# Kernel tuning notes

Hardware: AMD Instinct MI355X
Metric: run time of the kernel (lower is better)

## Reference

```python
import jax, jax.numpy as jnp
import numpy as np

B, SQ, SK, D, H = 2, 2048, 2048, 1024, 16
DK = D // H


def setup_inputs() -> dict:
    key = jax.random.key(0)
    ks = jax.random.split(key, 9)
    query = jax.random.normal(ks[0], (B, SQ, D), dtype=jnp.float32)
    k_in = jax.random.normal(ks[1], (B, SK, D), dtype=jnp.float32)
    v_in = jax.random.normal(ks[2], (B, SK, D), dtype=jnp.float32)
    # padding mask: 1 for valid tokens, 0 for padding; lengths in [SK//2, SK]
    lengths = jax.random.randint(ks[3], (B,), SK // 2, SK + 1)
    mask = (jnp.arange(SK)[None, :] < lengths[:, None]).astype(jnp.int32)
    scale = 1.0 / np.sqrt(D)
    Wq = jax.random.normal(ks[4], (D, D), dtype=jnp.float32) * scale
    Wk = jax.random.normal(ks[5], (D, D), dtype=jnp.float32) * scale
    Wv = jax.random.normal(ks[6], (D, D), dtype=jnp.float32) * scale
    Wo = jax.random.normal(ks[7], (D, D), dtype=jnp.float32) * scale
    return {"query": query, "key": k_in, "value": v_in, "mask": mask,
            "Wq": Wq, "Wk": Wk, "Wv": Wv, "Wo": Wo}


def reference(query, key, value, mask, Wq, Wk, Wv, Wo):
    # linear projections (torch Linear: x @ W.T)
    q = (query @ Wq.T).reshape(B, SQ, H, DK).transpose(0, 2, 1, 3)  # [B,H,SQ,DK]
    k = (key @ Wk.T).reshape(B, SK, H, DK).transpose(0, 2, 1, 3)    # [B,H,SK,DK]
    v = (value @ Wv.T).reshape(B, SK, H, DK).transpose(0, 2, 1, 3)  # [B,H,SK,DK]
    scores = jnp.einsum('bhqd,bhkd->bhqk', q, k) / jnp.sqrt(jnp.float32(DK))
    # padding mask: (B, SK) -> (B, 1, 1, SK)
    scores = jnp.where(mask[:, None, None, :] == 0, -jnp.inf, scores)
    # future (causal) mask
    future = jnp.triu(jnp.ones((SQ, SK), dtype=bool), k=1)
    scores = jnp.where(future[None, None], -jnp.inf, scores)
    attn = jax.nn.softmax(scores, axis=-1)
    attn = jnp.nan_to_num(attn, nan=0.0)
    ctx = jnp.einsum('bhqk,bhkd->bhqd', attn, v)
    ctx = ctx.transpose(0, 2, 1, 3).reshape(B, SQ, D)
    return ctx @ Wo.T
```

## Files before the change

### kernel.cpp

```cpp
#include <hip/hip_runtime.h>
#include <hip/hip_bf16.h>
#include <stdint.h>

#define BB 2
#define SS 2048
#define DD 1024
#define HH 16
#define DKK 64
#define MM (BB*SS)
#define LOG2E 1.4426950408889634f
#define QSCALE (0.125f * LOG2E)

typedef __attribute__((ext_vector_type(8))) short short8;
typedef __attribute__((ext_vector_type(4))) float f32x4;

__device__ __forceinline__ short bfr(float f) {
    return (short)((__float_as_uint(f) + 0x8000u) >> 16);
}

__device__ __forceinline__ short8 cvt8(float4 a, float4 b) {
    short8 s;
    s[0] = bfr(a.x); s[1] = bfr(a.y); s[2] = bfr(a.z); s[3] = bfr(a.w);
    s[4] = bfr(b.x); s[5] = bfr(b.y); s[6] = bfr(b.z); s[7] = bfr(b.w);
    return s;
}

__global__ __launch_bounds__(256) void qkv_gemm(const float* __restrict__ Aq,
                                                const float* __restrict__ Ak,
                                                const float* __restrict__ Av,
                                                const float* __restrict__ Wq,
                                                const float* __restrict__ Wk,
                                                const float* __restrict__ Wv,
                                                short* __restrict__ Qb,
                                                short* __restrict__ Kb,
                                                short* __restrict__ Vtb) {
    __shared__ __align__(16) short As[2][128][40];
    __shared__ __align__(16) short Ws[2][128][40];
    const int z = blockIdx.z;
    const float* A = (z == 0) ? Aq : (z == 1) ? Ak : Av;
    const float* W = (z == 0) ? Wq : (z == 1) ? Wk : Wv;
    short* Y = (z == 0) ? Qb : (z == 1) ? Kb : Vtb;

    const int t    = threadIdx.x;
    const int wave = t >> 6;
    const int lane = t & 63;
    const int la   = lane & 15;
    const int quad = lane >> 4;
    const int wm   = wave & 1;
    const int wn   = wave >> 1;
    const int m0   = blockIdx.x * 128;
    const int n0   = blockIdx.y * 128;

    const int srow = t >> 1;
    const int scol = (t & 1) * 16;

    f32x4 acc[4][4];
    #pragma unroll
    for (int i = 0; i < 4; ++i)
        #pragma unroll
        for (int j = 0; j < 4; ++j) acc[i][j] = {0.f, 0.f, 0.f, 0.f};

    float4 ar[4], wr[4];
    auto loadG = [&](int i) {
        const int k0 = i * 32;
        const float4* pa = (const float4*)(A + (size_t)(m0 + srow) * DD + k0 + scol);
        ar[0] = pa[0]; ar[1] = pa[1]; ar[2] = pa[2]; ar[3] = pa[3];
        const float4* pw = (const float4*)(W + (size_t)(n0 + srow) * DD + k0 + scol);
        wr[0] = pw[0]; wr[1] = pw[1]; wr[2] = pw[2]; wr[3] = pw[3];
    };
    auto storeL = [&](int buf) {
        *(short8*)&As[buf][srow][scol]     = cvt8(ar[0], ar[1]);
        *(short8*)&As[buf][srow][scol + 8] = cvt8(ar[2], ar[3]);
        *(short8*)&Ws[buf][srow][scol]     = cvt8(wr[0], wr[1]);
        *(short8*)&Ws[buf][srow][scol + 8] = cvt8(wr[2], wr[3]);
    };

    loadG(0);
    storeL(0);
    __syncthreads();

    const int NIT = DD / 32;
    for (int i = 0; i < NIT; ++i) {
        if (i + 1 < NIT) loadG(i + 1);
        const int buf = i & 1;
        short8 af[4], bfv[4];
        #pragma unroll
        for (int mt = 0; mt < 4; ++mt)
            af[mt] = *(const short8*)&As[buf][wm * 64 + mt * 16 + la][quad * 8];
        #pragma unroll
        for (int nt = 0; nt < 4; ++nt)
            bfv[nt] = *(const short8*)&Ws[buf][wn * 64 + nt * 16 + la][quad * 8];
        #pragma unroll
        for (int mt = 0; mt < 4; ++mt)
            #pragma unroll
            for (int nt = 0; nt < 4; ++nt)
                acc[mt][nt] = __builtin_amdgcn_mfma_f32_16x16x32_bf16(af[mt], bfv[nt], acc[mt][nt], 0, 0, 0);
        if (i + 1 < NIT) {
            storeL((i + 1) & 1);
            __syncthreads();
        }
    }

    #pragma unroll
    for (int mt = 0; mt < 4; ++mt) {
        #pragma unroll
        for (int nt = 0; nt < 4; ++nt) {
            #pragma unroll
            for (int r = 0; r < 4; ++r) {
                const int m = m0 + wm * 64 + mt * 16 + quad * 4 + r;
                const int n = n0 + wn * 64 + nt * 16 + la;
                const int b = m >> 11, s = m & (SS - 1);
                const int h = n >> 6,  dk = n & (DKK - 1);
                float v = acc[mt][nt][r];
                if (z == 0) {
                    Y[(((size_t)(b * HH + h) * SS + s) * DKK) + dk] = bfr(v * QSCALE);
                } else if (z == 1) {
                    Y[(((size_t)(b * HH + h) * SS + s) * DKK) + dk] = bfr(v);
                } else {
                    Y[(((size_t)(b * HH + h) * DKK + dk) * SS) + s] = bfr(v);
                }
            }
        }
    }
}

__global__ __launch_bounds__(256) void attn_fused(const short* __restrict__ Q,
                                                  const short* __restrict__ K,
                                                  const short* __restrict__ Vt,
                                                  const int* __restrict__ mask,
                                                  short* __restrict__ ctx) {
    const int b = blockIdx.z, h = blockIdx.y, x = blockIdx.x;
    const int t = threadIdx.x, wave = t >> 6, lane = t & 63;
    const int la = lane & 15, quad = lane >> 4;

    __shared__ __align__(16) short Ks[2][64][72];
    __shared__ __align__(16) short Vs[2][64][72];
    __shared__ __align__(16) short Ps[64][72];

    const size_t kbase = ((size_t)(b * HH + h) * SS) * DKK;
    const size_t vbase = ((size_t)(b * HH + h) * DKK) * SS;

    const int srow = t >> 2;
    const int scol = (t & 3) * 16;
    short8 kr[2], vr[2];

    auto loadG = [&](int kt) {
        const short* kp = K + kbase + (size_t)(kt * 64 + srow) * DKK + scol;
        kr[0] = ((const short8*)kp)[0]; kr[1] = ((const short8*)kp)[1];
        const short* vp = Vt + vbase + (size_t)srow * SS + kt * 64 + scol;
        vr[0] = ((const short8*)vp)[0]; vr[1] = ((const short8*)vp)[1];
    };
    auto storeL = [&](int buf) {
        *(short8*)&Ks[buf][srow][scol]     = kr[0];
        *(short8*)&Ks[buf][srow][scol + 8] = kr[1];
        *(short8*)&Vs[buf][srow][scol]     = vr[0];
        *(short8*)&Vs[buf][srow][scol + 8] = vr[1];
    };

    #pragma unroll 1
    for (int phase = 0; phase < 2; ++phase) {
        const int qt = phase ? x : (31 - x);
        const size_t qbase = kbase + (size_t)(qt * 64) * DKK;
        const short8 aq0 = *(const short8*)(Q + qbase + (size_t)(wave * 16 + la) * DKK + quad * 8);
        const short8 aq1 = *(const short8*)(Q + qbase + (size_t)(wave * 16 + la) * DKK + 32 + quad * 8);

        float rs[4] = {0.f, 0.f, 0.f, 0.f};
        f32x4 o[4];
        #pragma unroll
        for (int dc = 0; dc < 4; ++dc) o[dc] = {0.f, 0.f, 0.f, 0.f};

        const int nkt = qt + 1;
        loadG(0);
        storeL(0);
        __syncthreads();

        for (int kt = 0; kt < nkt; ++kt) {
            if (kt + 1 < nkt) loadG(kt + 1);
            const int buf = kt & 1;
            const bool diag   = (kt == qt);
            const bool padded = (kt >= SS / 128);

            f32x4 s[4];
            #pragma unroll
            for (int ct = 0; ct < 4; ++ct) {
                s[ct] = {0.f, 0.f, 0.f, 0.f};
                short8 kb0 = *(const short8*)&Ks[buf][ct * 16 + la][quad * 8];
                short8 kb1 = *(const short8*)&Ks[buf][ct * 16 + la][32 + quad * 8];
                s[ct] = __builtin_amdgcn_mfma_f32_16x16x32_bf16(aq0, kb0, s[ct], 0, 0, 0);
                s[ct] = __builtin_amdgcn_mfma_f32_16x16x32_bf16(aq1, kb1, s[ct], 0, 0, 0);
            }

            const int rowq = qt * 64 + wave * 16 + quad * 4;
            #pragma unroll
            for (int ct = 0; ct < 4; ++ct) {
                const int col = kt * 64 + ct * 16 + la;
                const int mv = padded ? mask[b * SS + col] : 1;
                #pragma unroll
                for (int r = 0; r < 4; ++r) {
                    const bool dead = (diag && col > rowq + r) || (padded && mv == 0);
                    const float p = dead ? 0.f : exp2f(s[ct][r]);
                    rs[r] += p;
                    Ps[wave * 16 + quad * 4 + r][ct * 16 + la] = bfr(p);
                }
            }

            #pragma unroll
            for (int c2 = 0; c2 < 2; ++c2) {
                short8 pa = *(const short8*)&Ps[wave * 16 + la][c2 * 32 + quad * 8];
                #pragma unroll
                for (int dc = 0; dc < 4; ++dc) {
                    short8 vb = *(const short8*)&Vs[buf][dc * 16 + la][c2 * 32 + quad * 8];
                    o[dc] = __builtin_amdgcn_mfma_f32_16x16x32_bf16(pa, vb, o[dc], 0, 0, 0);
                }
            }

            if (kt + 1 < nkt) {
                storeL((kt + 1) & 1);
                __syncthreads();
            }
        }

        #pragma unroll
        for (int r = 0; r < 4; ++r) {
            float v = rs[r];
            v += __shfl_xor(v, 1, 64);
            v += __shfl_xor(v, 2, 64);
            v += __shfl_xor(v, 4, 64);
            v += __shfl_xor(v, 8, 64);
            const float inv = 1.0f / v;
            const int q = qt * 64 + wave * 16 + quad * 4 + r;
            #pragma unroll
            for (int dc = 0; dc < 4; ++dc) {
                const int d = dc * 16 + la;
                ctx[((size_t)(b * SS + q) * DD) + h * DKK + d] = bfr(o[dc][r] * inv);
            }
        }
        __syncthreads();
    }
}

__global__ __launch_bounds__(256) void o_gemm(const short* __restrict__ Ctx,
                                              const float* __restrict__ Wo,
                                              float* __restrict__ out) {
    __shared__ __align__(16) short As[2][128][40];
    __shared__ __align__(16) short Ws[2][64][40];
    const int t    = threadIdx.x;
    const int wave = t >> 6;
    const int lane = t & 63;
    const int la   = lane & 15;
    const int quad = lane >> 4;
    const int wm   = wave & 1;
    const int wn   = wave >> 1;
    const int m0   = blockIdx.x * 128;
    const int n0   = blockIdx.y * 64;

    const int srowA = t >> 1;
    const int scolA = (t & 1) * 16;
    const int srowW = t >> 2;
    const int scolW = (t & 3) * 8;

    f32x4 acc[4][2];
    #pragma unroll
    for (int i = 0; i < 4; ++i)
        #pragma unroll
        for (int j = 0; j < 2; ++j) acc[i][j] = {0.f, 0.f, 0.f, 0.f};

    short8 ab[2];
    float4 wr[2];
    auto loadG = [&](int i) {
        const int k0 = i * 32;
        const short8* pa = (const short8*)(Ctx + (size_t)(m0 + srowA) * DD + k0 + scolA);
        ab[0] = pa[0]; ab[1] = pa[1];
        const float4* pw = (const float4*)(Wo + (size_t)(n0 + srowW) * DD + k0 + scolW);
        wr[0] = pw[0]; wr[1] = pw[1];
    };
    auto storeL = [&](int buf) {
        *(short8*)&As[buf][srowA][scolA]     = ab[0];
        *(short8*)&As[buf][srowA][scolA + 8] = ab[1];
        *(short8*)&Ws[buf][srowW][scolW]     = cvt8(wr[0], wr[1]);
    };

    loadG(0);
    storeL(0);
    __syncthreads();

    const int NIT = DD / 32;
    for (int i = 0; i < NIT; ++i) {
        if (i + 1 < NIT) loadG(i + 1);
        const int buf = i & 1;
        short8 af[4], bfv[2];
        #pragma unroll
        for (int mt = 0; mt < 4; ++mt)
            af[mt] = *(const short8*)&As[buf][wm * 64 + mt * 16 + la][quad * 8];
        #pragma unroll
        for (int nt = 0; nt < 2; ++nt)
            bfv[nt] = *(const short8*)&Ws[buf][wn * 32 + nt * 16 + la][quad * 8];
        #pragma unroll
        for (int mt = 0; mt < 4; ++mt)
            #pragma unroll
            for (int nt = 0; nt < 2; ++nt)
                acc[mt][nt] = __builtin_amdgcn_mfma_f32_16x16x32_bf16(af[mt], bfv[nt], acc[mt][nt], 0, 0, 0);
        if (i + 1 < NIT) {
            storeL((i + 1) & 1);
            __syncthreads();
        }
    }

    #pragma unroll
    for (int mt = 0; mt < 4; ++mt) {
        #pragma unroll
        for (int nt = 0; nt < 2; ++nt) {
            #pragma unroll
            for (int r = 0; r < 4; ++r) {
                const int m = m0 + wm * 64 + mt * 16 + quad * 4 + r;
                const int n = n0 + wn * 32 + nt * 16 + la;
                out[(size_t)m * DD + n] = acc[mt][nt][r];
            }
        }
    }
}

extern "C" void kernel_launch(void* const* d_in, const int* in_sizes, int n_in,
                              void* d_out, int out_size, void* d_ws, size_t ws_size,
                              hipStream_t stream) {
    (void)in_sizes; (void)n_in; (void)out_size; (void)ws_size;
    const float* query = (const float*)d_in[0];
    const float* key   = (const float*)d_in[1];
    const float* value = (const float*)d_in[2];
    const int*   mask  = (const int*)  d_in[3];
    const float* Wq    = (const float*)d_in[4];
    const float* Wk    = (const float*)d_in[5];
    const float* Wv    = (const float*)d_in[6];
    const float* Wo    = (const float*)d_in[7];

    short* Qb  = (short*)d_ws;
    short* Kb  = Qb + (size_t)BB * HH * SS * DKK;
    short* Vtb = Kb + (size_t)BB * HH * SS * DKK;
    short* Ctx = Vtb + (size_t)BB * HH * SS * DKK;

    dim3 tb(256);

    dim3 gq(MM / 128, DD / 128, 3);
    hipLaunchKernelGGL(qkv_gemm, gq, tb, 0, stream, query, key, value, Wq, Wk, Wv,
                       Qb, Kb, Vtb);

    dim3 ga(SS / 128, HH, BB);
    hipLaunchKernelGGL(attn_fused, ga, tb, 0, stream, (const short*)Qb, (const short*)Kb,
                       (const short*)Vtb, mask, Ctx);

    dim3 go(MM / 128, DD / 64);
    hipLaunchKernelGGL(o_gemm, go, tb, 0, stream, (const short*)Ctx, Wo, (float*)d_out);
}
```

Before: 257.0 us.

## Add bf16 pre-conversion pass and direct global-to-LDS loads with pre-padded K/V tiles

Adds a pass that converts all fp32 activations and weights to bf16 in one sweep. The GEMMs then load tiles straight into LDS with global_load_lds, with no register staging or in-loop conversion. The QKV projection writes K and V in pre-padded 64x72 tile layouts so the attention kernel can copy each tile to LDS directly. Attention now uses 128-thread blocks, each wave handling 32 query rows. The new path drops double buffering and only runs when the workspace is large enough, trading an extra full read and write of the inputs for cheaper inner loops.

```diff
diff --git a/kernel.cpp b/kernel.cpp
--- a/kernel.cpp
+++ b/kernel.cpp
@@ -17,12 +17,279 @@
 __device__ __forceinline__ short bfr(float f) {
     return (short)((__float_as_uint(f) + 0x8000u) >> 16);
 }
-
 __device__ __forceinline__ short8 cvt8(float4 a, float4 b) {
     short8 s;
     s[0] = bfr(a.x); s[1] = bfr(a.y); s[2] = bfr(a.z); s[3] = bfr(a.w);
     s[4] = bfr(b.x); s[5] = bfr(b.y); s[6] = bfr(b.z); s[7] = bfr(b.w);
     return s;
+}
+
+__device__ __forceinline__ void dma16(const void* g, void* l) {
+    __builtin_amdgcn_global_load_lds(
+        (const __attribute__((address_space(1))) uint32_t*)g,
+        (__attribute__((address_space(3))) uint32_t*)(uintptr_t)l, 16, 0, 0);
+}
+
+
+__global__ __launch_bounds__(256) void cvt_all(const float* __restrict__ q,
+                                               const float* __restrict__ k,
+                                               const float* __restrict__ v,
+                                               const float* __restrict__ wq,
+                                               const float* __restrict__ wk,
+                                               const float* __restrict__ wv,
+                                               const float* __restrict__ wo,
+                                               short* __restrict__ dst) {
+    const size_t nth = (size_t)gridDim.x * blockDim.x;
+    const size_t tid = (size_t)blockIdx.x * blockDim.x + threadIdx.x;
+    for (size_t i8 = tid; i8 < (1u << 21); i8 += nth) {
+        const size_t e = i8 * 8;
+        const float* s;
+        size_t rel;
+        if (e < 4194304)        { s = q; rel = e; }
+        else if (e < 8388608)   { s = k; rel = e - 4194304; }
+        else if (e < 12582912)  { s = v; rel = e - 8388608; }
+        else {
+            const size_t we = e - 12582912;
+            s = (we < 1048576) ? wq : (we < 2097152) ? wk : (we < 3145728) ? wv : wo;
+            rel = we & 1048575;
+        }
+        const float4* p = (const float4*)(s + rel);
+        *(short8*)(dst + e) = cvt8(p[0], p[1]);
+    }
+}
+
+__global__ __launch_bounds__(256) void qkv_lds(const short* __restrict__ Abf,
+                                               const short* __restrict__ Wbf,
+                                               short* __restrict__ Qb,
+                                               short* __restrict__ Kp,
+                                               short* __restrict__ Vp) {
+    __shared__ __align__(16) short As[128 * 32];
+    __shared__ __align__(16) short Ws[128 * 32];
+    const int z = blockIdx.z;
+    const short* A = Abf + (size_t)z * 4194304;
+    const short* W = Wbf + (size_t)z * 1048576;
+    const int t = threadIdx.x, wave = t >> 6, lane = t & 63;
+    const int la = lane & 15, quad = lane >> 4;
+    const int wm = wave & 1, wn = wave >> 1;
+    const int m0 = blockIdx.x * 128, n0 = blockIdx.y * 128;
+
+    f32x4 acc[4][4];
+    #pragma unroll
+    for (int i = 0; i < 4; ++i)
+        #pragma unroll
+        for (int j = 0; j < 4; ++j) acc[i][j] = {0.f, 0.f, 0.f, 0.f};
+
+    const int c0 = t, c1 = 256 + t;
+
+    for (int k0 = 0; k0 < DD; k0 += 32) {
+        dma16(A + (size_t)(m0 + (c0 >> 2)) * DD + k0 + (c0 & 3) * 8, (short*)As + c0 * 8);
+        dma16(A + (size_t)(m0 + (c1 >> 2)) * DD + k0 + (c1 & 3) * 8, (short*)As + c1 * 8);
+        dma16(W + (size_t)(n0 + (c0 >> 2)) * DD + k0 + (c0 & 3) * 8, (short*)Ws + c0 * 8);
+        dma16(W + (size_t)(n0 + (c1 >> 2)) * DD + k0 + (c1 & 3) * 8, (short*)Ws + c1 * 8);
+        __syncthreads();
+        short8 af[4], bf[4];
+        #pragma unroll
+        for (int mt = 0; mt < 4; ++mt)
+            af[mt] = *(const short8*)&As[(wm * 64 + mt * 16 + la) * 32 + quad * 8];
+        #pragma unroll
+        for (int nt = 0; nt < 4; ++nt)
+            bf[nt] = *(const short8*)&Ws[(wn * 64 + nt * 16 + la) * 32 + quad * 8];
+        #pragma unroll
+        for (int mt = 0; mt < 4; ++mt)
+            #pragma unroll
+            for (int nt = 0; nt < 4; ++nt)
+                acc[mt][nt] = __builtin_amdgcn_mfma_f32_16x16x32_bf16(af[mt], bf[nt], acc[mt][nt], 0, 0, 0);
+        __syncthreads();
+    }
+
+    #pragma unroll
+    for (int mt = 0; mt < 4; ++mt) {
+        #pragma unroll
+        for (int nt = 0; nt < 4; ++nt) {
+            #pragma unroll
+            for (int r = 0; r < 4; ++r) {
+                const int m = m0 + wm * 64 + mt * 16 + quad * 4 + r;
+                const int n = n0 + wn * 64 + nt * 16 + la;
+                const int b = m >> 11, s = m & (SS - 1);
+                const int h = n >> 6,  dk = n & 63;
+                const int bh = b * HH + h;
+                const float v = acc[mt][nt][r];
+                if (z == 0) {
+                    Qb[((size_t)bh * SS + s) * DKK + dk] = bfr(v * QSCALE);
+                } else if (z == 1) {
+                    Kp[((size_t)(bh * 32 + (s >> 6)) * 64 + (s & 63)) * 72 + dk] = bfr(v);
+                } else {
+                    Vp[((size_t)(bh * 32 + (s >> 6)) * 64 + dk) * 72 + (s & 63)] = bfr(v);
+                }
+            }
+        }
+    }
+}
+
+__global__ __launch_bounds__(128) void attn2(const short* __restrict__ Q,
+                                             const short* __restrict__ Kp,
+                                             const short* __restrict__ Vp,
+                                             const int* __restrict__ mask,
+                                             short* __restrict__ ctx) {
+    const int b = blockIdx.z, h = blockIdx.y, x = blockIdx.x;
+    const int t = threadIdx.x, wave = t >> 6, lane = t & 63;
+    const int la = lane & 15, quad = lane >> 4;
+    const int bh = b * HH + h;
+
+    __shared__ __align__(16) short Ks[64 * 72];
+    __shared__ __align__(16) short Vs[64 * 72];
+    __shared__ __align__(16) short Ps[64 * 72];
+
+    const short* Kt0 = Kp + (size_t)bh * 32 * 4608;
+    const short* Vt0 = Vp + (size_t)bh * 32 * 4608;
+
+    #pragma unroll 1
+    for (int phase = 0; phase < 2; ++phase) {
+        const int qt = phase ? x : (31 - x);
+        short8 aq[2][2];
+        #pragma unroll
+        for (int mt = 0; mt < 2; ++mt)
+            #pragma unroll
+            for (int hf = 0; hf < 2; ++hf)
+                aq[mt][hf] = *(const short8*)(Q + ((size_t)bh * SS + qt * 64 + wave * 32 + mt * 16 + la) * DKK
+                                              + hf * 32 + quad * 8);
+
+        float rs[2][4] = {};
+        f32x4 o[2][4];
+        #pragma unroll
+        for (int mt = 0; mt < 2; ++mt)
+            #pragma unroll
+            for (int dc = 0; dc < 4; ++dc) o[mt][dc] = {0.f, 0.f, 0.f, 0.f};
+
+        for (int kt = 0; kt <= qt; ++kt) {
+            {
+                const short* src = (wave == 0) ? (Kt0 + (size_t)kt * 4608) : (Vt0 + (size_t)kt * 4608);
+                short* dst = (wave == 0) ? Ks : Vs;
+                #pragma unroll
+                for (int j = 0; j < 9; ++j)
+                    dma16(src + j * 512 + lane * 8, dst + j * 512 + lane * 8);
+            }
+            __syncthreads();
+
+            f32x4 s[2][4];
+            #pragma unroll
+            for (int mt = 0; mt < 2; ++mt)
+                #pragma unroll
+                for (int ct = 0; ct < 4; ++ct) s[mt][ct] = {0.f, 0.f, 0.f, 0.f};
+            #pragma unroll
+            for (int ct = 0; ct < 4; ++ct) {
+                short8 kb0 = *(const short8*)&Ks[(ct * 16 + la) * 72 + quad * 8];
+                short8 kb1 = *(const short8*)&Ks[(ct * 16 + la) * 72 + 32 + quad * 8];
+                #pragma unroll
+                for (int mt = 0; mt < 2; ++mt) {
+                    s[mt][ct] = __builtin_amdgcn_mfma_f32_16x16x32_bf16(aq[mt][0], kb0, s[mt][ct], 0, 0, 0);
+                    s[mt][ct] = __builtin_amdgcn_mfma_f32_16x16x32_bf16(aq[mt][1], kb1, s[mt][ct], 0, 0, 0);
+                }
+            }
+
+            const bool diag   = (kt == qt);
+            const bool padded = (kt >= 16);
+            #pragma unroll
+            for (int ct = 0; ct < 4; ++ct) {
+                const int col = kt * 64 + ct * 16 + la;
+                const int mv = padded ? mask[b * SS + col] : 1;
+                #pragma unroll
+                for (int mt = 0; mt < 2; ++mt) {
+                    const int row0 = qt * 64 + wave * 32 + mt * 16 + quad * 4;
+                    #pragma unroll
+                    for (int r = 0; r < 4; ++r) {
+                        const bool dead = (diag && col > row0 + r) || (padded && mv == 0);
+                        const float p = dead ? 0.f : exp2f(s[mt][ct][r]);
+                        rs[mt][r] += p;
+                        Ps[(wave * 32 + mt * 16 + quad * 4 + r) * 72 + ct * 16 + la] = bfr(p);
+                    }
+                }
+            }
+
+            #pragma unroll
+            for (int c2 = 0; c2 < 2; ++c2) {
+                short8 pa[2];
+                #pragma unroll
+                for (int mt = 0; mt < 2; ++mt)
+                    pa[mt] = *(const short8*)&Ps[(wave * 32 + mt * 16 + la) * 72 + c2 * 32 + quad * 8];
+                #pragma unroll
+                for (int dc = 0; dc < 4; ++dc) {
+                    short8 vb = *(const short8*)&Vs[(dc * 16 + la) * 72 + c2 * 32 + quad * 8];
+                    #pragma unroll
+                    for (int mt = 0; mt < 2; ++mt)
+                        o[mt][dc] = __builtin_amdgcn_mfma_f32_16x16x32_bf16(pa[mt], vb, o[mt][dc], 0, 0, 0);
+                }
+            }
+            __syncthreads();
+        }
+
+        #pragma unroll
+        for (int mt = 0; mt < 2; ++mt) {
+            #pragma unroll
+            for (int r = 0; r < 4; ++r) {
+                float v = rs[mt][r];
+                v += __shfl_xor(v, 1, 64);
+                v += __shfl_xor(v, 2, 64);
+                v += __shfl_xor(v, 4, 64);
+                v += __shfl_xor(v, 8, 64);
+                const float inv = 1.0f / v;
+                const int qq = qt * 64 + wave * 32 + mt * 16 + quad * 4 + r;
+                #pragma unroll
+                for (int dc = 0; dc < 4; ++dc)
+                    ctx[((size_t)(b * SS + qq) * DD) + h * DKK + dc * 16 + la] = bfr(o[mt][dc][r] * inv);
+            }
+        }
+    }
+}
+
+__global__ __launch_bounds__(256) void o_lds(const short* __restrict__ Ctx,
+                                             const short* __restrict__ Wob,
+                                             float* __restrict__ out) {
+    __shared__ __align__(16) short As[128 * 32];
+    __shared__ __align__(16) short Ws[64 * 32];
+    const int t = threadIdx.x, wave = t >> 6, lane = t & 63;
+    const int la = lane & 15, quad = lane >> 4;
+    const int wm = wave & 1, wn = wave >> 1;
+    const int m0 = blockIdx.x * 128, n0 = blockIdx.y * 64;
+
+    f32x4 acc[4][2];
+    #pragma unroll
+    for (int i = 0; i < 4; ++i)
+        #pragma unroll
+        for (int j = 0; j < 2; ++j) acc[i][j] = {0.f, 0.f, 0.f, 0.f};
+
+    const int c0 = t, c1 = 256 + t;
+
+    for (int k0 = 0; k0 < DD; k0 += 32) {
+        dma16(Ctx + (size_t)(m0 + (c0 >> 2)) * DD + k0 + (c0 & 3) * 8, (short*)As + c0 * 8);
+        dma16(Ctx + (size_t)(m0 + (c1 >> 2)) * DD + k0 + (c1 & 3) * 8, (short*)As + c1 * 8);
+        dma16(Wob + (size_t)(n0 + (t >> 2)) * DD + k0 + (t & 3) * 8, (short*)Ws + t * 8);
+        __syncthreads();
+        short8 af[4], bf[2];
+        #pragma unroll
+        for (int mt = 0; mt < 4; ++mt)
+            af[mt] = *(const short8*)&As[(wm * 64 + mt * 16 + la) * 32 + quad * 8];
+        #pragma unroll
+        for (int nt = 0; nt < 2; ++nt)
+            bf[nt] = *(const short8*)&Ws[(wn * 32 + nt * 16 + la) * 32 + quad * 8];
+        #pragma unroll
+        for (int mt = 0; mt < 4; ++mt)
+            #pragma unroll
+            for (int nt = 0; nt < 2; ++nt)
+                acc[mt][nt] = __builtin_amdgcn_mfma_f32_16x16x32_bf16(af[mt], bf[nt], acc[mt][nt], 0, 0, 0);
+        __syncthreads();
+    }
+
+    #pragma unroll
+    for (int mt = 0; mt < 4; ++mt)
+        #pragma unroll
+        for (int nt = 0; nt < 2; ++nt)
+            #pragma unroll
+            for (int r = 0; r < 4; ++r) {
+                const int m = m0 + wm * 64 + mt * 16 + quad * 4 + r;
+                const int n = n0 + wn * 32 + nt * 16 + la;
+                out[(size_t)m * DD + n] = acc[mt][nt][r];
+            }
 }
 
 __global__ __launch_bounds__(256) void qkv_gemm(const float* __restrict__ Aq,
@@ -40,26 +307,16 @@
     const float* A = (z == 0) ? Aq : (z == 1) ? Ak : Av;
     const float* W = (z == 0) ? Wq : (z == 1) ? Wk : Wv;
     short* Y = (z == 0) ? Qb : (z == 1) ? Kb : Vtb;
-
-    const int t    = threadIdx.x;
-    const int wave = t >> 6;
-    const int lane = t & 63;
-    const int la   = lane & 15;
-    const int quad = lane >> 4;
-    const int wm   = wave & 1;
-    const int wn   = wave >> 1;
-    const int m0   = blockIdx.x * 128;
-    const int n0   = blockIdx.y * 128;
-
-    const int srow = t >> 1;
-    const int scol = (t & 1) * 16;
-
+    const int t = threadIdx.x, wave = t >> 6, lane = t & 63;
+    const int la = lane & 15, quad = lane >> 4;
+    const int wm = wave & 1, wn = wave >> 1;
+    const int m0 = blockIdx.x * 128, n0 = blockIdx.y * 128;
+    const int srow = t >> 1, scol = (t & 1) * 16;
     f32x4 acc[4][4];
     #pragma unroll
     for (int i = 0; i < 4; ++i)
         #pragma unroll
         for (int j = 0; j < 4; ++j) acc[i][j] = {0.f, 0.f, 0.f, 0.f};
-
     float4 ar[4], wr[4];
     auto loadG = [&](int i) {
         const int k0 = i * 32;
@@ -74,11 +331,7 @@
         *(short8*)&Ws[buf][srow][scol]     = cvt8(wr[0], wr[1]);
         *(short8*)&Ws[buf][srow][scol + 8] = cvt8(wr[2], wr[3]);
     };
-
-    loadG(0);
-    storeL(0);
-    __syncthreads();
-
+    loadG(0); storeL(0); __syncthreads();
     const int NIT = DD / 32;
     for (int i = 0; i < NIT; ++i) {
         if (i + 1 < NIT) loadG(i + 1);
@@ -95,33 +348,23 @@
             #pragma unroll
             for (int nt = 0; nt < 4; ++nt)
                 acc[mt][nt] = __builtin_amdgcn_mfma_f32_16x16x32_bf16(af[mt], bfv[nt], acc[mt][nt], 0, 0, 0);
-        if (i + 1 < NIT) {
-            storeL((i + 1) & 1);
-            __syncthreads();
-        }
-    }
-
-    #pragma unroll
-    for (int mt = 0; mt < 4; ++mt) {
-        #pragma unroll
-        for (int nt = 0; nt < 4; ++nt) {
+        if (i + 1 < NIT) { storeL((i + 1) & 1); __syncthreads(); }
+    }
+    #pragma unroll
+    for (int mt = 0; mt < 4; ++mt)
+        #pragma unroll
+        for (int nt = 0; nt < 4; ++nt)
             #pragma unroll
             for (int r = 0; r < 4; ++r) {
                 const int m = m0 + wm * 64 + mt * 16 + quad * 4 + r;
                 const int n = n0 + wn * 64 + nt * 16 + la;
                 const int b = m >> 11, s = m & (SS - 1);
-                const int h = n >> 6,  dk = n & (DKK - 1);
+                const int h = n >> 6, dk = n & 63;
                 float v = acc[mt][nt][r];
-                if (z == 0) {
-                    Y[(((size_t)(b * HH + h) * SS + s) * DKK) + dk] = bfr(v * QSCALE);
-                } else if (z == 1) {
-                    Y[(((size_t)(b * HH + h) * SS + s) * DKK) + dk] = bfr(v);
-                } else {
-                    Y[(((size_t)(b * HH + h) * DKK + dk) * SS) + s] = bfr(v);
-                }
-            }
-        }
-    }
+                if (z == 0)      Y[(((size_t)(b * HH + h) * SS + s) * DKK) + dk] = bfr(v * QSCALE);
+                else if (z == 1) Y[(((size_t)(b * HH + h) * SS + s) * DKK) + dk] = bfr(v);
+                else             Y[(((size_t)(b * HH + h) * DKK + dk) * SS) + s] = bfr(v);
+            }
 }
 
 __global__ __launch_bounds__(256) void attn_fused(const short* __restrict__ Q,
@@ -132,18 +375,13 @@
     const int b = blockIdx.z, h = blockIdx.y, x = blockIdx.x;
     const int t = threadIdx.x, wave = t >> 6, lane = t & 63;
     const int la = lane & 15, quad = lane >> 4;
-
     __shared__ __align__(16) short Ks[2][64][72];
     __shared__ __align__(16) short Vs[2][64][72];
     __shared__ __align__(16) short Ps[64][72];
-
     const size_t kbase = ((size_t)(b * HH + h) * SS) * DKK;
     const size_t vbase = ((size_t)(b * HH + h) * DKK) * SS;
-
-    const int srow = t >> 2;
-    const int scol = (t & 3) * 16;
+    const int srow = t >> 2, scol = (t & 3) * 16;
     short8 kr[2], vr[2];
-
     auto loadG = [&](int kt) {
         const short* kp = K + kbase + (size_t)(kt * 64 + srow) * DKK + scol;
         kr[0] = ((const short8*)kp)[0]; kr[1] = ((const short8*)kp)[1];
@@ -156,30 +394,23 @@
         *(short8*)&Vs[buf][srow][scol]     = vr[0];
         *(short8*)&Vs[buf][srow][scol + 8] = vr[1];
     };
-
     #pragma unroll 1
     for (int phase = 0; phase < 2; ++phase) {
         const int qt = phase ? x : (31 - x);
         const size_t qbase = kbase + (size_t)(qt * 64) * DKK;
         const short8 aq0 = *(const short8*)(Q + qbase + (size_t)(wave * 16 + la) * DKK + quad * 8);
         const short8 aq1 = *(const short8*)(Q + qbase + (size_t)(wave * 16 + la) * DKK + 32 + quad * 8);
-
         float rs[4] = {0.f, 0.f, 0.f, 0.f};
         f32x4 o[4];
         #pragma unroll
         for (int dc = 0; dc < 4; ++dc) o[dc] = {0.f, 0.f, 0.f, 0.f};
-
         const int nkt = qt + 1;
-        loadG(0);
-        storeL(0);
-        __syncthreads();
-
+        loadG(0); storeL(0); __syncthreads();
         for (int kt = 0; kt < nkt; ++kt) {
             if (kt + 1 < nkt) loadG(kt + 1);
             const int buf = kt & 1;
-            const bool diag   = (kt == qt);
-            const bool padded = (kt >= SS / 128);
-
+            const bool diag = (kt == qt);
+            const bool padded = (kt >= 16);
             f32x4 s[4];
             #pragma unroll
             for (int ct = 0; ct < 4; ++ct) {
@@ -189,7 +420,6 @@
                 s[ct] = __builtin_amdgcn_mfma_f32_16x16x32_bf16(aq0, kb0, s[ct], 0, 0, 0);
                 s[ct] = __builtin_amdgcn_mfma_f32_16x16x32_bf16(aq1, kb1, s[ct], 0, 0, 0);
             }
-
             const int rowq = qt * 64 + wave * 16 + quad * 4;
             #pragma unroll
             for (int ct = 0; ct < 4; ++ct) {
@@ -203,7 +433,6 @@
                     Ps[wave * 16 + quad * 4 + r][ct * 16 + la] = bfr(p);
                 }
             }
-
             #pragma unroll
             for (int c2 = 0; c2 < 2; ++c2) {
                 short8 pa = *(const short8*)&Ps[wave * 16 + la][c2 * 32 + quad * 8];
@@ -213,13 +442,8 @@
                     o[dc] = __builtin_amdgcn_mfma_f32_16x16x32_bf16(pa, vb, o[dc], 0, 0, 0);
                 }
             }
-
-            if (kt + 1 < nkt) {
-                storeL((kt + 1) & 1);
-                __syncthreads();
-            }
+            if (kt + 1 < nkt) { storeL((kt + 1) & 1); __syncthreads(); }
         }
-
         #pragma unroll
         for (int r = 0; r < 4; ++r) {
             float v = rs[r];
@@ -230,10 +454,8 @@
             const float inv = 1.0f / v;
             const int q = qt * 64 + wave * 16 + quad * 4 + r;
             #pragma unroll
-            for (int dc = 0; dc < 4; ++dc) {
-                const int d = dc * 16 + la;
-                ctx[((size_t)(b * SS + q) * DD) + h * DKK + d] = bfr(o[dc][r] * inv);
-            }
+            for (int dc = 0; dc < 4; ++dc)
+                ctx[((size_t)(b * SS + q) * DD) + h * DKK + dc * 16 + la] = bfr(o[dc][r] * inv);
         }
         __syncthreads();
     }
@@ -244,27 +466,17 @@
                                               float* __restrict__ out) {
     __shared__ __align__(16) short As[2][128][40];
     __shared__ __align__(16) short Ws[2][64][40];
-    const int t    = threadIdx.x;
-    const int wave = t >> 6;
-    const int lane = t & 63;
-    const int la   = lane & 15;
-    const int quad = lane >> 4;
-    const int wm   = wave & 1;
-    const int wn   = wave >> 1;
-    const int m0   = blockIdx.x * 128;
-    const int n0   = blockIdx.y * 64;
-
-    const int srowA = t >> 1;
-    const int scolA = (t & 1) * 16;
-    const int srowW = t >> 2;
-    const int scolW = (t & 3) * 8;
-
+    const int t = threadIdx.x, wave = t >> 6, lane = t & 63;
+    const int la = lane & 15, quad = lane >> 4;
+    const int wm = wave & 1, wn = wave >> 1;
+    const int m0 = blockIdx.x * 128, n0 = blockIdx.y * 64;
+    const int srowA = t >> 1, scolA = (t & 1) * 16;
+    const int srowW = t >> 2, scolW = (t & 3) * 8;
     f32x4 acc[4][2];
     #pragma unroll
     for (int i = 0; i < 4; ++i)
         #pragma unroll
         for (int j = 0; j < 2; ++j) acc[i][j] = {0.f, 0.f, 0.f, 0.f};
-
     short8 ab[2];
     float4 wr[2];
     auto loadG = [&](int i) {
@@ -279,11 +491,7 @@
         *(short8*)&As[buf][srowA][scolA + 8] = ab[1];
         *(short8*)&Ws[buf][srowW][scolW]     = cvt8(wr[0], wr[1]);
     };
-
-    loadG(0);
-    storeL(0);
-    __syncthreads();
-
+    loadG(0); storeL(0); __syncthreads();
     const int NIT = DD / 32;
     for (int i = 0; i < NIT; ++i) {
         if (i + 1 < NIT) loadG(i + 1);
@@ -300,30 +508,24 @@
             #pragma unroll
             for (int nt = 0; nt < 2; ++nt)
                 acc[mt][nt] = __builtin_amdgcn_mfma_f32_16x16x32_bf16(af[mt], bfv[nt], acc[mt][nt], 0, 0, 0);
-        if (i + 1 < NIT) {
-            storeL((i + 1) & 1);
-            __syncthreads();
-        }
-    }
-
-    #pragma unroll
-    for (int mt = 0; mt < 4; ++mt) {
-        #pragma unroll
-        for (int nt = 0; nt < 2; ++nt) {
+        if (i + 1 < NIT) { storeL((i + 1) & 1); __syncthreads(); }
+    }
+    #pragma unroll
+    for (int mt = 0; mt < 4; ++mt)
+        #pragma unroll
+        for (int nt = 0; nt < 2; ++nt)
             #pragma unroll
             for (int r = 0; r < 4; ++r) {
                 const int m = m0 + wm * 64 + mt * 16 + quad * 4 + r;
                 const int n = n0 + wn * 32 + nt * 16 + la;
                 out[(size_t)m * DD + n] = acc[mt][nt][r];
             }
-        }
-    }
 }
 
 extern "C" void kernel_launch(void* const* d_in, const int* in_sizes, int n_in,
                               void* d_out, int out_size, void* d_ws, size_t ws_size,
                               hipStream_t stream) {
-    (void)in_sizes; (void)n_in; (void)out_size; (void)ws_size;
+    (void)in_sizes; (void)n_in; (void)out_size;
     const float* query = (const float*)d_in[0];
     const float* key   = (const float*)d_in[1];
     const float* value = (const float*)d_in[2];
@@ -332,22 +534,33 @@
     const float* Wk    = (const float*)d_in[5];
     const float* Wv    = (const float*)d_in[6];
     const float* Wo    = (const float*)d_in[7];
-
-    short* Qb  = (short*)d_ws;
-    short* Kb  = Qb + (size_t)BB * HH * SS * DKK;
-    short* Vtb = Kb + (size_t)BB * HH * SS * DKK;
-    short* Ctx = Vtb + (size_t)BB * HH * SS * DKK;
-
     dim3 tb(256);
 
-    dim3 gq(MM / 128, DD / 128, 3);
-    hipLaunchKernelGGL(qkv_gemm, gq, tb, 0, stream, query, key, value, Wq, Wk, Wv,
-                       Qb, Kb, Vtb);
-
-    dim3 ga(SS / 128, HH, BB);
-    hipLaunchKernelGGL(attn_fused, ga, tb, 0, stream, (const short*)Qb, (const short*)Kb,
-                       (const short*)Vtb, mask, Ctx);
-
-    dim3 go(MM / 128, DD / 64);
-    hipLaunchKernelGGL(o_gemm, go, tb, 0, stream, (const short*)Ctx, Wo, (float*)d_out);
-}
+    if (ws_size >= (size_t)61000000) {
+        short* Abf = (short*)d_ws;
+        short* Wbf = Abf + 12582912;
+        short* Qb  = Abf + 16777216;
+        short* Kp  = Abf + 20971520;
+        short* Vp  = Abf + 25690112;
+        short* Ctx = Abf;
+
+        hipLaunchKernelGGL(cvt_all, dim3(1024), tb, 0, stream,
+                           query, key, value, Wq, Wk, Wv, Wo, Abf);
+        hipLaunchKernelGGL(qkv_lds, dim3(32, 8, 3), tb, 0, stream, Abf, Wbf, Qb, Kp, Vp);
+        hipLaunchKernelGGL(attn2, dim3(16, 16, 2), dim3(128), 0, stream,
+                           (const short*)Qb, (const short*)Kp, (const short*)Vp, mask, Ctx);
+        hipLaunchKernelGGL(o_lds, dim3(32, 16), tb, 0, stream,
+                           (const short*)Ctx, (const short*)(Wbf + 3145728), (float*)d_out);
+    } else {
+        short* Qb  = (short*)d_ws;
+        short* Kb  = Qb + (size_t)BB * HH * SS * DKK;
+        short* Vtb = Kb + (size_t)BB * HH * SS * DKK;
+        short* Ctx = Vtb + (size_t)BB * HH * SS * DKK;
+        hipLaunchKernelGGL(qkv_gemm, dim3(MM / 128, DD / 128, 3), tb, 0, stream,
+                           query, key, value, Wq, Wk, Wv, Qb, Kb, Vtb);
+        hipLaunchKernelGGL(attn_fused, dim3(SS / 128, HH, BB), tb, 0, stream,
+                           (const short*)Qb, (const short*)Kb, (const short*)Vtb, mask, Ctx);
+        hipLaunchKernelGGL(o_gemm, dim3(MM / 128, DD / 64), tb, 0, stream,
+                           (const short*)Ctx, Wo, (float*)d_out);
+    }
+}
```

Result: no change. 255.9 us (-0.4%).
